# Kernel tuning notes

Measured on AMD Instinct MI355X. Metric: run time of the kernel, lower is better.

## Reference

```python
import jax, jax.numpy as jnp
import numpy as np
from jax import lax

INPUT_DIM = 16
H1, H2 = 64, 32
OUT_DIM = 1
B, T = 4096, 168


def _uniform(key, shape, k):
    return jax.random.uniform(key, shape, jnp.float32, -k, k)


def setup_inputs() -> dict:
    key = jax.random.key(0)
    ks = jax.random.split(key, 12)
    k1 = 1.0 / np.sqrt(H1)
    k2 = 1.0 / np.sqrt(H2)
    return {
        "x": jax.random.normal(ks[0], (B, T, INPUT_DIM), jnp.float32),
        # layer 1 (PyTorch gate order: i, f, g, o)
        "W_ih1": _uniform(ks[1], (4 * H1, INPUT_DIM), k1),
        "W_hh1": _uniform(ks[2], (4 * H1, H1), k1),
        "b_ih1": _uniform(ks[3], (4 * H1,), k1),
        "b_hh1": _uniform(ks[4], (4 * H1,), k1),
        # layer 2
        "W_ih2": _uniform(ks[5], (4 * H2, H1), k2),
        "W_hh2": _uniform(ks[6], (4 * H2, H2), k2),
        "b_ih2": _uniform(ks[7], (4 * H2,), k2),
        "b_hh2": _uniform(ks[8], (4 * H2,), k2),
        # final linear
        "W_fc": _uniform(ks[9], (OUT_DIM, H2), k2),
        "b_fc": _uniform(ks[10], (OUT_DIM,), k2),
    }


def _lstm(x, W_ih, W_hh, b_ih, b_hh, hidden):
    # Precompute input-to-gate projections for all timesteps: [B, T, 4H]
    xg = jnp.einsum("btd,gd->btg", x, W_ih) + b_ih + b_hh

    def step(carry, xt):
        h, c = carry
        gates = xt + h @ W_hh.T  # [B, 4H]
        i, f, g, o = jnp.split(gates, 4, axis=-1)
        i = jax.nn.sigmoid(i)
        f = jax.nn.sigmoid(f)
        g = jnp.tanh(g)
        o = jax.nn.sigmoid(o)
        c = f * c + i * g
        h = o * jnp.tanh(c)
        return (h, c), h

    bsz = x.shape[0]
    init = (jnp.zeros((bsz, hidden), x.dtype), jnp.zeros((bsz, hidden), x.dtype))
    (_, _), hs = lax.scan(step, init, jnp.swapaxes(xg, 0, 1))  # hs: [T, B, H]
    return jnp.swapaxes(hs, 0, 1)  # [B, T, H]


def reference(x, W_ih1, W_hh1, b_ih1, b_hh1, W_ih2, W_hh2, b_ih2, b_hh2, W_fc, b_fc):
    # Dropout layers are identity at inference (p=0.2 in train only).
    h1 = _lstm(x, W_ih1, W_hh1, b_ih1, b_hh1, H1)   # [B, T, 64]
    h2 = _lstm(h1, W_ih2, W_hh2, b_ih2, b_hh2, H2)  # [B, T, 32]
    last = h2[:, -1, :]                              # [B, 32]
    return last @ W_fc.T + b_fc                      # [B, OUT_DIM]
```

## Files before the change

### kernel.cpp

```cpp
#include <hip/hip_runtime.h>


typedef __bf16 bf16x8 __attribute__((ext_vector_type(8)));
typedef float  f32x4  __attribute__((ext_vector_type(4)));

constexpr int T_SEQ = 168;
constexpr int NB    = 16;

__device__ __forceinline__ float fsig(float v)  { return __builtin_amdgcn_rcpf(1.f + __expf(-v)); }
__device__ __forceinline__ float ftanhf(float v){ return 2.f * __builtin_amdgcn_rcpf(1.f + __expf(-2.f * v)) - 1.f; }

__device__ __forceinline__ void split_bf16(float x, __bf16& hi, __bf16& lo) {
  hi = (__bf16)x;
  lo = (__bf16)(x - (float)hi);
}

__device__ __forceinline__ void load_frag8(const float* __restrict__ Wrow, int k0,
                                           bf16x8& hi, bf16x8& lo) {
#pragma unroll
  for (int j = 0; j < 8; ++j) {
    float v = Wrow[k0 + j];
    __bf16 h = (__bf16)v;
    hi[j] = h;
    lo[j] = (__bf16)(v - (float)h);
  }
}

#define MFMA(a, b, c) __builtin_amdgcn_mfma_f32_16x16x32_bf16((a), (b), (c), 0, 0, 0)

__global__ __launch_bounds__(512, 1)
void lstm_mfma_kernel(const float* __restrict__ x,
    const float* __restrict__ Wih1, const float* __restrict__ Whh1,
    const float* __restrict__ bih1, const float* __restrict__ bhh1,
    const float* __restrict__ Wih2, const float* __restrict__ Whh2,
    const float* __restrict__ bih2, const float* __restrict__ bhh2,
    const float* __restrict__ Wfc,  const float* __restrict__ bfc,
    float* __restrict__ out)
{
  __shared__ __align__(16) __bf16 sA1[2][4 * 64 * 8];
  __shared__ __align__(16) __bf16 sA2[2][2 * 64 * 8];
  __shared__ __align__(16) __bf16 sW2[8 * 4 * 64 * 8];
  __shared__ __align__(16) __bf16 sWh2[2 * 4 * 2 * 64 * 8];
  __shared__ __align__(16) float  sP[2][2 * 4 * 64 * 4];
  __shared__ __align__(16) float  sH2f[16 * 32];

  const int tid  = threadIdx.x;
  const int w    = tid >> 6;
  const int lane = tid & 63;
  const int q    = lane >> 4;
  const int col  = lane & 15;
  const int b0   = blockIdx.x * NB;

  const bool isL1  = (w < 4);
  const bool isL2b = (w == 4) || (w == 5);
  const bool isL2a = (w >= 6);
  const int  wl2b  = w - 4;
  const int  wl2a  = w - 6;

  bf16x8 bhh[4][4];
  bf16x8 bih[4];
  float  b1v[4] = {0.f, 0.f, 0.f, 0.f};
  if (isL1) {
#pragma unroll
    for (int g = 0; g < 4; ++g) {
      const int r = g * 64 + w * 16 + col;
      const float* Wr = Whh1 + r * 64;
      bf16x8 h0, l0, h1f, l1f;
      load_frag8(Wr, 0 * 32 + q * 8, h0, l0);
      load_frag8(Wr, 1 * 32 + q * 8, h1f, l1f);
      bhh[g][0] = h0; bhh[g][1] = h1f; bhh[g][2] = l0; bhh[g][3] = l1f;
      bf16x8 xh, xl;
      load_frag8(Wih1 + r * 16, (q & 1) * 8, xh, xl);
      bih[g] = (q < 2) ? xh : xl;
      b1v[g] = bih1[r] + bhh1[r];
    }
  }
  float b2v[4] = {0.f, 0.f, 0.f, 0.f};
  if (isL2b) {
#pragma unroll
    for (int g = 0; g < 4; ++g) {
      const int r = g * 32 + wl2b * 16 + col;
      b2v[g] = bih2[r] + bhh2[r];
    }
  }

  for (int idx = tid; idx < 8 * 4 * 64; idx += 512) {
    const int nt = idx >> 8;
    const int kb = (idx >> 6) & 3;
    const int ln = idx & 63;
    const int qq = ln >> 4, cc = ln & 15;
    const int g  = nt >> 1, wv = nt & 1;
    const int r  = g * 32 + wv * 16 + cc;
    const int k0 = (kb & 1) * 32 + qq * 8;
    bf16x8 hh, ll;
    load_frag8(Wih2 + r * 64, k0, hh, ll);
    *(bf16x8*)&sW2[((nt * 4 + kb) * 64 + ln) * 8] = (kb < 2) ? hh : ll;
  }
  for (int idx = tid; idx < 2 * 4 * 2 * 64; idx += 512) {
    const int ln = idx & 63;
    const int hl = (idx >> 6) & 1;
    const int g  = (idx >> 7) & 3;
    const int wl = idx >> 9;
    const int qq = ln >> 4, cc = ln & 15;
    const int r  = g * 32 + wl * 16 + cc;
    bf16x8 hh, ll;
    load_frag8(Whh2 + r * 32, qq * 8, hh, ll);
    *(bf16x8*)&sWh2[(((wl * 4 + g) * 2 + hl) * 64 + ln) * 8] = hl ? ll : hh;
  }

  {
    bf16x8 z;
#pragma unroll
    for (int j = 0; j < 8; ++j) z[j] = (__bf16)0.f;
    for (int i = tid; i < 2 * 4 * 64; i += 512) *(bf16x8*)&sA1[0][i * 8] = z;
    for (int i = tid; i < 2 * 2 * 64; i += 512) *(bf16x8*)&sA2[0][i * 8] = z;
  }
  __syncthreads();

  const float* xbase = x + ((size_t)(b0 + col) * T_SEQ) * 16 + (q & 1) * 8;
  float4 xcA, xcB, xnA, xnB;
  if (isL1) {
    xcA = *(const float4*)(xbase + 0);
    xcB = *(const float4*)(xbase + 4);
  }

  float c1s[4] = {0.f, 0.f, 0.f, 0.f};
  float c2s[4] = {0.f, 0.f, 0.f, 0.f};
  const int uu   = w * 16 + col;
  const int uu2b = wl2b * 16 + col;

  const int kbh  = uu >> 5;
  const int lnb  = ((uu & 31) >> 3) * 16;
  const int jj   = uu & 7;
  const int lnb2 = ((uu2b & 31) >> 3) * 16;
  const int jj2  = uu2b & 7;

#define STEP(Pc, DO_L1, DO_XPRE, DO_L2A, DO_L2B, DO_H2F, TT) do {              \
    if ((DO_XPRE) && isL1) {                                                   \
      const float* xr = xbase + (size_t)((TT) + 1) * 16;                       \
      xnA = *(const float4*)(xr + 0);                                          \
      xnB = *(const float4*)(xr + 4);                                          \
    }                                                                          \
    if ((DO_L1) && isL1) {                                                     \
      const float xc[8] = {xcA.x, xcA.y, xcA.z, xcA.w, xcB.x, xcB.y, xcB.z, xcB.w}; \
      bf16x8 xh8, xl8;                                                         \
      _Pragma("unroll")                                                        \
      for (int j = 0; j < 8; ++j) {                                            \
        __bf16 h_, l_; split_bf16(xc[j], h_, l_);                              \
        xh8[j] = h_; xl8[j] = l_;                                              \
      }                                                                        \
      const bf16x8 ax0 = (q < 2) ? xh8 : xl8;                                  \
      const bf16x8 ax1 = (q < 2) ? xl8 : xh8;                                  \
      bf16x8 a1[4];                                                            \
      _Pragma("unroll")                                                        \
      for (int kb = 0; kb < 4; ++kb)                                           \
        a1[kb] = *(const bf16x8*)&sA1[(Pc)][(kb * 64 + lane) * 8];             \
      f32x4 c[4];                                                              \
      _Pragma("unroll")                                                        \
      for (int g = 0; g < 4; ++g) { c[g][0] = b1v[g]; c[g][1] = b1v[g]; c[g][2] = b1v[g]; c[g][3] = b1v[g]; } \
      _Pragma("unroll")                                                        \
      for (int g = 0; g < 4; ++g) {                                            \
        c[g] = MFMA(ax0,   bih[g],    c[g]);                                   \
        c[g] = MFMA(ax1,   bih[g],    c[g]);                                   \
        c[g] = MFMA(a1[0], bhh[g][0], c[g]);                                   \
        c[g] = MFMA(a1[1], bhh[g][1], c[g]);                                   \
        c[g] = MFMA(a1[2], bhh[g][0], c[g]);                                   \
        c[g] = MFMA(a1[3], bhh[g][1], c[g]);                                   \
        c[g] = MFMA(a1[0], bhh[g][2], c[g]);                                   \
        c[g] = MFMA(a1[1], bhh[g][3], c[g]);                                   \
      }                                                                        \
      _Pragma("unroll")                                                        \
      for (int r = 0; r < 4; ++r) {                                            \
        const float iv = fsig(c[0][r]);                                        \
        const float fv = fsig(c[1][r]);                                        \
        const float gv = ftanhf(c[2][r]);                                      \
        const float ov = fsig(c[3][r]);                                        \
        const float cc = fmaf(fv, c1s[r], iv * gv);                            \
        c1s[r] = cc;                                                           \
        __bf16 hh_, hl_;                                                       \
        split_bf16(ov * ftanhf(cc), hh_, hl_);                                 \
        const int m = q * 4 + r;                                               \
        sA1[1 - (Pc)][((kbh * 64) + lnb + m) * 8 + jj]       = hh_;            \
        sA1[1 - (Pc)][(((2 + kbh) * 64) + lnb + m) * 8 + jj] = hl_;            \
      }                                                                        \
      if (DO_XPRE) { xcA = xnA; xcB = xnB; }                                   \
    }                                                                          \
    if ((DO_L2A) && isL2a) {                                                   \
      bf16x8 a2[4];                                                            \
      _Pragma("unroll")                                                        \
      for (int kb = 0; kb < 4; ++kb)                                           \
        a2[kb] = *(const bf16x8*)&sA1[(Pc)][(kb * 64 + lane) * 8];             \
      _Pragma("unroll")                                                        \
      for (int g = 0; g < 4; ++g) {                                            \
        const int nt = g * 2 + wl2a;                                           \
        const bf16x8 bb0 = *(const bf16x8*)&sW2[((nt * 4 + 0) * 64 + lane) * 8]; \
        const bf16x8 bb1 = *(const bf16x8*)&sW2[((nt * 4 + 1) * 64 + lane) * 8]; \
        const bf16x8 bb2 = *(const bf16x8*)&sW2[((nt * 4 + 2) * 64 + lane) * 8]; \
        const bf16x8 bb3 = *(const bf16x8*)&sW2[((nt * 4 + 3) * 64 + lane) * 8]; \
        f32x4 pa = {0.f, 0.f, 0.f, 0.f};                                       \
        pa = MFMA(a2[0], bb0, pa);                                             \
        pa = MFMA(a2[1], bb1, pa);                                             \
        pa = MFMA(a2[0], bb2, pa);                                             \
        pa = MFMA(a2[1], bb3, pa);                                             \
        pa = MFMA(a2[2], bb0, pa);                                             \
        pa = MFMA(a2[3], bb1, pa);                                             \
        *(f32x4*)&sP[(Pc)][((wl2a * 4 + g) * 64 + lane) * 4] = pa;             \
      }                                                                        \
    }                                                                          \
    if ((DO_L2B) && isL2b) {                                                   \
      const bf16x8 ah0 = *(const bf16x8*)&sA2[1 - (Pc)][(0 * 64 + lane) * 8];  \
      const bf16x8 ah1 = *(const bf16x8*)&sA2[1 - (Pc)][(1 * 64 + lane) * 8];  \
      f32x4 c2[4];                                                             \
      _Pragma("unroll")                                                        \
      for (int g = 0; g < 4; ++g) {                                            \
        const bf16x8 whh = *(const bf16x8*)&sWh2[(((wl2b * 4 + g) * 2 + 0) * 64 + lane) * 8]; \
        const bf16x8 whl = *(const bf16x8*)&sWh2[(((wl2b * 4 + g) * 2 + 1) * 64 + lane) * 8]; \
        c2[g][0] = b2v[g]; c2[g][1] = b2v[g]; c2[g][2] = b2v[g]; c2[g][3] = b2v[g]; \
        c2[g] = MFMA(ah0, whh, c2[g]);                                         \
        c2[g] = MFMA(ah1, whh, c2[g]);                                         \
        c2[g] = MFMA(ah0, whl, c2[g]);                                         \
        c2[g] += *(const f32x4*)&sP[1 - (Pc)][((wl2b * 4 + g) * 64 + lane) * 4]; \
      }                                                                        \
      _Pragma("unroll")                                                        \
      for (int r = 0; r < 4; ++r) {                                            \
        const float iv = fsig(c2[0][r]);                                       \
        const float fv = fsig(c2[1][r]);                                       \
        const float gv = ftanhf(c2[2][r]);                                     \
        const float ov = fsig(c2[3][r]);                                       \
        const float cc = fmaf(fv, c2s[r], iv * gv);                            \
        c2s[r] = cc;                                                           \
        const float hf = ov * ftanhf(cc);                                      \
        __bf16 hh_, hl_;                                                       \
        split_bf16(hf, hh_, hl_);                                              \
        const int m = q * 4 + r;                                               \
        sA2[(Pc)][((0 * 64) + lnb2 + m) * 8 + jj2] = hh_;                      \
        sA2[(Pc)][((1 * 64) + lnb2 + m) * 8 + jj2] = hl_;                      \
        if (DO_H2F) sH2f[m * 32 + uu2b] = hf;                                  \
      }                                                                        \
    }                                                                          \
    __syncthreads();                                                           \
  } while (0)

  STEP(0, true,  true,  false, false, false, 0);
  STEP(1, true,  true,  true,  false, false, 1);
  for (int t = 2; t < 166; t += 2) {
    STEP(0, true, true, true, true, false, t);
    STEP(1, true, true, true, true, false, t + 1);
  }
  STEP(0, true,  true,  true,  true,  false, 166);
  STEP(1, true,  false, true,  true,  false, 167);
  STEP(0, false, false, true,  true,  false, 168);
  STEP(1, false, false, false, true,  true,  169);
#undef STEP

  if (tid < NB) {
    float s = bfc[0];
#pragma unroll
    for (int j = 0; j < 32; ++j) s = fmaf(Wfc[j], sH2f[tid * 32 + j], s);
    out[b0 + tid] = s;
  }
}

extern "C" void kernel_launch(void* const* d_in, const int* in_sizes, int n_in,
                              void* d_out, int out_size, void* d_ws, size_t ws_size,
                              hipStream_t stream) {
  (void)in_sizes; (void)n_in; (void)out_size; (void)d_ws; (void)ws_size;
  const float* x    = (const float*)d_in[0];
  const float* Wih1 = (const float*)d_in[1];
  const float* Whh1 = (const float*)d_in[2];
  const float* bih1 = (const float*)d_in[3];
  const float* bhh1 = (const float*)d_in[4];
  const float* Wih2 = (const float*)d_in[5];
  const float* Whh2 = (const float*)d_in[6];
  const float* bih2 = (const float*)d_in[7];
  const float* bhh2 = (const float*)d_in[8];
  const float* Wfc  = (const float*)d_in[9];
  const float* bfc  = (const float*)d_in[10];
  float* out = (float*)d_out;

  hipLaunchKernelGGL(lstm_mfma_kernel, dim3(4096 / NB), dim3(512), 0, stream,
                     x, Wih1, Whh1, bih1, bhh1, Wih2, Whh2, bih2, bhh2, Wfc, bfc, out);
}
```

Baseline: 292.6 us.

## Keep layer-2 weights in registers, split L1 MFMA chains, allow two waves

Layer-2 recurrent weights (hi/lo) and the hi half of the layer-2 input weights now live in registers instead of LDS, so only the lo half stays in shared memory. This cuts LDS reads on the serial critical path and shrinks LDS use, which together with waves_per_eu(2,2) may let two blocks share a CU. The layer-1 gate accumulation is split into two independent MFMA chains to shorten the dependency latency, and the LDS h-load is moved ahead of the x prefetch. The cost is more VGPRs under a tighter register budget for two waves per EU, which risks spilling.

Result: faster. 273.5 us (-6.5%).

```diff
diff --git a/kernel.cpp b/kernel.cpp
--- a/kernel.cpp
+++ b/kernel.cpp
@@ -28,7 +28,7 @@
 
 #define MFMA(a, b, c) __builtin_amdgcn_mfma_f32_16x16x32_bf16((a), (b), (c), 0, 0, 0)
 
-__global__ __launch_bounds__(512, 1)
+__global__ __launch_bounds__(512) __attribute__((amdgpu_waves_per_eu(2, 2)))
 void lstm_mfma_kernel(const float* __restrict__ x,
     const float* __restrict__ Wih1, const float* __restrict__ Whh1,
     const float* __restrict__ bih1, const float* __restrict__ bhh1,
@@ -39,8 +39,7 @@
 {
   __shared__ __align__(16) __bf16 sA1[2][4 * 64 * 8];
   __shared__ __align__(16) __bf16 sA2[2][2 * 64 * 8];
-  __shared__ __align__(16) __bf16 sW2[8 * 4 * 64 * 8];
-  __shared__ __align__(16) __bf16 sWh2[2 * 4 * 2 * 64 * 8];
+  __shared__ __align__(16) __bf16 sW2lo[8 * 2 * 64 * 8];
   __shared__ __align__(16) float  sP[2][2 * 4 * 64 * 4];
   __shared__ __align__(16) float  sH2f[16 * 32];
 
@@ -75,37 +74,43 @@
       b1v[g] = bih1[r] + bhh1[r];
     }
   }
-  float b2v[4] = {0.f, 0.f, 0.f, 0.f};
+  bf16x8 wh2h[4], wh2l[4];
+  float  b2v[4] = {0.f, 0.f, 0.f, 0.f};
   if (isL2b) {
 #pragma unroll
     for (int g = 0; g < 4; ++g) {
       const int r = g * 32 + wl2b * 16 + col;
+      bf16x8 hh, ll;
+      load_frag8(Whh2 + r * 32, q * 8, hh, ll);
+      wh2h[g] = hh; wh2l[g] = ll;
       b2v[g] = bih2[r] + bhh2[r];
     }
   }
-
-  for (int idx = tid; idx < 8 * 4 * 64; idx += 512) {
-    const int nt = idx >> 8;
-    const int kb = (idx >> 6) & 3;
-    const int ln = idx & 63;
-    const int qq = ln >> 4, cc = ln & 15;
-    const int g  = nt >> 1, wv = nt & 1;
-    const int r  = g * 32 + wv * 16 + cc;
-    const int k0 = (kb & 1) * 32 + qq * 8;
+  bf16x8 w2ih[4][2];
+  if (isL2a) {
+#pragma unroll
+    for (int g = 0; g < 4; ++g) {
+      const int r = g * 32 + wl2a * 16 + col;
+#pragma unroll
+      for (int kb = 0; kb < 2; ++kb) {
+        bf16x8 hh, ll;
+        load_frag8(Wih2 + r * 64, kb * 32 + q * 8, hh, ll);
+        w2ih[g][kb] = hh;
+      }
+    }
+  }
+
+  for (int idx = tid; idx < 8 * 2 * 64; idx += 512) {
+    const int nt  = idx >> 7;
+    const int kb2 = (idx >> 6) & 1;
+    const int ln  = idx & 63;
+    const int qq  = ln >> 4, cc = ln & 15;
+    const int g   = nt >> 1, wv = nt & 1;
+    const int r   = g * 32 + wv * 16 + cc;
+    const int k0  = kb2 * 32 + qq * 8;
     bf16x8 hh, ll;
     load_frag8(Wih2 + r * 64, k0, hh, ll);
-    *(bf16x8*)&sW2[((nt * 4 + kb) * 64 + ln) * 8] = (kb < 2) ? hh : ll;
-  }
-  for (int idx = tid; idx < 2 * 4 * 2 * 64; idx += 512) {
-    const int ln = idx & 63;
-    const int hl = (idx >> 6) & 1;
-    const int g  = (idx >> 7) & 3;
-    const int wl = idx >> 9;
-    const int qq = ln >> 4, cc = ln & 15;
-    const int r  = g * 32 + wl * 16 + cc;
-    bf16x8 hh, ll;
-    load_frag8(Whh2 + r * 32, qq * 8, hh, ll);
-    *(bf16x8*)&sWh2[(((wl * 4 + g) * 2 + hl) * 64 + ln) * 8] = hl ? ll : hh;
+    *(bf16x8*)&sW2lo[((nt * 2 + kb2) * 64 + ln) * 8] = ll;
   }
 
   {
@@ -136,12 +141,16 @@
   const int jj2  = uu2b & 7;
 
 #define STEP(Pc, DO_L1, DO_XPRE, DO_L2A, DO_L2B, DO_H2F, TT) do {              \
-    if ((DO_XPRE) && isL1) {                                                   \
-      const float* xr = xbase + (size_t)((TT) + 1) * 16;                       \
-      xnA = *(const float4*)(xr + 0);                                          \
-      xnB = *(const float4*)(xr + 4);                                          \
-    }                                                                          \
     if ((DO_L1) && isL1) {                                                     \
+      bf16x8 a1[4];                                                            \
+      _Pragma("unroll")                                                        \
+      for (int kb = 0; kb < 4; ++kb)                                           \
+        a1[kb] = *(const bf16x8*)&sA1[(Pc)][(kb * 64 + lane) * 8];             \
+      if (DO_XPRE) {                                                           \
+        const float* xr = xbase + (size_t)((TT) + 1) * 16;                     \
+        xnA = *(const float4*)(xr + 0);                                        \
+        xnB = *(const float4*)(xr + 4);                                        \
+      }                                                                        \
       const float xc[8] = {xcA.x, xcA.y, xcA.z, xcA.w, xcB.x, xcB.y, xcB.z, xcB.w}; \
       bf16x8 xh8, xl8;                                                         \
       _Pragma("unroll")                                                        \
@@ -151,30 +160,29 @@
       }                                                                        \
       const bf16x8 ax0 = (q < 2) ? xh8 : xl8;                                  \
       const bf16x8 ax1 = (q < 2) ? xl8 : xh8;                                  \
-      bf16x8 a1[4];                                                            \
-      _Pragma("unroll")                                                        \
-      for (int kb = 0; kb < 4; ++kb)                                           \
-        a1[kb] = *(const bf16x8*)&sA1[(Pc)][(kb * 64 + lane) * 8];             \
-      f32x4 c[4];                                                              \
-      _Pragma("unroll")                                                        \
-      for (int g = 0; g < 4; ++g) { c[g][0] = b1v[g]; c[g][1] = b1v[g]; c[g][2] = b1v[g]; c[g][3] = b1v[g]; } \
-      _Pragma("unroll")                                                        \
-      for (int g = 0; g < 4; ++g) {                                            \
-        c[g] = MFMA(ax0,   bih[g],    c[g]);                                   \
-        c[g] = MFMA(ax1,   bih[g],    c[g]);                                   \
-        c[g] = MFMA(a1[0], bhh[g][0], c[g]);                                   \
-        c[g] = MFMA(a1[1], bhh[g][1], c[g]);                                   \
-        c[g] = MFMA(a1[2], bhh[g][0], c[g]);                                   \
-        c[g] = MFMA(a1[3], bhh[g][1], c[g]);                                   \
-        c[g] = MFMA(a1[0], bhh[g][2], c[g]);                                   \
-        c[g] = MFMA(a1[1], bhh[g][3], c[g]);                                   \
+      f32x4 ca[4], cb[4];                                                      \
+      _Pragma("unroll")                                                        \
+      for (int g = 0; g < 4; ++g) {                                            \
+        ca[g][0] = b1v[g]; ca[g][1] = b1v[g]; ca[g][2] = b1v[g]; ca[g][3] = b1v[g]; \
+        cb[g][0] = 0.f; cb[g][1] = 0.f; cb[g][2] = 0.f; cb[g][3] = 0.f;        \
+      }                                                                        \
+      _Pragma("unroll")                                                        \
+      for (int g = 0; g < 4; ++g) {                                            \
+        ca[g] = MFMA(ax0,   bih[g],    ca[g]);                                 \
+        ca[g] = MFMA(ax1,   bih[g],    ca[g]);                                 \
+        ca[g] = MFMA(a1[0], bhh[g][0], ca[g]);                                 \
+        ca[g] = MFMA(a1[1], bhh[g][1], ca[g]);                                 \
+        cb[g] = MFMA(a1[2], bhh[g][0], cb[g]);                                 \
+        cb[g] = MFMA(a1[3], bhh[g][1], cb[g]);                                 \
+        cb[g] = MFMA(a1[0], bhh[g][2], cb[g]);                                 \
+        cb[g] = MFMA(a1[1], bhh[g][3], cb[g]);                                 \
       }                                                                        \
       _Pragma("unroll")                                                        \
       for (int r = 0; r < 4; ++r) {                                            \
-        const float iv = fsig(c[0][r]);                                        \
-        const float fv = fsig(c[1][r]);                                        \
-        const float gv = ftanhf(c[2][r]);                                      \
-        const float ov = fsig(c[3][r]);                                        \
+        const float iv = fsig(ca[0][r] + cb[0][r]);                            \
+        const float fv = fsig(ca[1][r] + cb[1][r]);                            \
+        const float gv = ftanhf(ca[2][r] + cb[2][r]);                          \
+        const float ov = fsig(ca[3][r] + cb[3][r]);                            \
         const float cc = fmaf(fv, c1s[r], iv * gv);                            \
         c1s[r] = cc;                                                           \
         __bf16 hh_, hl_;                                                       \
@@ -193,17 +201,15 @@
       _Pragma("unroll")                                                        \
       for (int g = 0; g < 4; ++g) {                                            \
         const int nt = g * 2 + wl2a;                                           \
-        const bf16x8 bb0 = *(const bf16x8*)&sW2[((nt * 4 + 0) * 64 + lane) * 8]; \
-        const bf16x8 bb1 = *(const bf16x8*)&sW2[((nt * 4 + 1) * 64 + lane) * 8]; \
-        const bf16x8 bb2 = *(const bf16x8*)&sW2[((nt * 4 + 2) * 64 + lane) * 8]; \
-        const bf16x8 bb3 = *(const bf16x8*)&sW2[((nt * 4 + 3) * 64 + lane) * 8]; \
+        const bf16x8 bb2 = *(const bf16x8*)&sW2lo[((nt * 2 + 0) * 64 + lane) * 8]; \
+        const bf16x8 bb3 = *(const bf16x8*)&sW2lo[((nt * 2 + 1) * 64 + lane) * 8]; \
         f32x4 pa = {0.f, 0.f, 0.f, 0.f};                                       \
-        pa = MFMA(a2[0], bb0, pa);                                             \
-        pa = MFMA(a2[1], bb1, pa);                                             \
-        pa = MFMA(a2[0], bb2, pa);                                             \
+        pa = MFMA(a2[0], w2ih[g][0], pa);                         \
+        pa = MFMA(a2[1], w2ih[g][1], pa);                                      \
+        pa = MFMA(a2[0], bb2, pa);                                \
         pa = MFMA(a2[1], bb3, pa);                                             \
-        pa = MFMA(a2[2], bb0, pa);                                             \
-        pa = MFMA(a2[3], bb1, pa);                                             \
+        pa = MFMA(a2[2], w2ih[g][0], pa);                         \
+        pa = MFMA(a2[3], w2ih[g][1], pa);                                      \
         *(f32x4*)&sP[(Pc)][((wl2a * 4 + g) * 64 + lane) * 4] = pa;             \
       }                                                                        \
     }                                                                          \
@@ -213,12 +219,10 @@
       f32x4 c2[4];                                                             \
       _Pragma("unroll")                                                        \
       for (int g = 0; g < 4; ++g) {                                            \
-        const bf16x8 whh = *(const bf16x8*)&sWh2[(((wl2b * 4 + g) * 2 + 0) * 64 + lane) * 8]; \
-        const bf16x8 whl = *(const bf16x8*)&sWh2[(((wl2b * 4 + g) * 2 + 1) * 64 + lane) * 8]; \
         c2[g][0] = b2v[g]; c2[g][1] = b2v[g]; c2[g][2] = b2v[g]; c2[g][3] = b2v[g]; \
-        c2[g] = MFMA(ah0, whh, c2[g]);                                         \
-        c2[g] = MFMA(ah1, whh, c2[g]);                                         \
-        c2[g] = MFMA(ah0, whl, c2[g]);                                         \
+        c2[g] = MFMA(ah0, wh2h[g], c2[g]);                                     \
+        c2[g] = MFMA(ah1, wh2h[g], c2[g]);                                     \
+        c2[g] = MFMA(ah0, wh2l[g], c2[g]);                                     \
         c2[g] += *(const f32x4*)&sP[1 - (Pc)][((wl2b * 4 + g) * 64 + lane) * 4]; \
       }                                                                        \
       _Pragma("unroll")                                                        \
```
